# Kernel optimization log

Measured on AMD Instinct MI355X. Metric: run time of the kernel, lower is better.

## Reference

```python
import jax, jax.numpy as jnp
import numpy as np

B, S, D, H = 4, 2048, 512, 8
HD = D // H  # head dim = 64


def setup_inputs() -> dict:
    key = jax.random.key(0)
    ks = jax.random.split(key, 7)
    s = 0.02
    return {
        "X": jax.random.normal(ks[0], (B, S, D), dtype=jnp.float32),
        "Y": jax.random.normal(ks[1], (B, S, D), dtype=jnp.float32),
        "Z": jax.random.normal(ks[2], (B, S, D), dtype=jnp.float32),
        # weights stored as [in, out] (torch Linear weight transposed)
        "Wq": jax.random.normal(ks[3], (D, D), dtype=jnp.float32) * s,
        "Wk": jax.random.normal(ks[4], (D, D), dtype=jnp.float32) * s,
        "Wv": jax.random.normal(ks[5], (D, D), dtype=jnp.float32) * s,  # dead in original forward
        "Wo": jax.random.normal(ks[6], (D, D), dtype=jnp.float32) * s,
    }


def _split_heads(t):
    # [B, S, D] -> [B, H, S, HD]
    return t.reshape(B, S, H, HD).transpose(0, 2, 1, 3)


def reference(X, Y, Z, Wq, Wk, Wv, Wo):
    q = _split_heads(X @ Wq)
    k = _split_heads(Y @ Wk)
    # NOTE: original module (faithfully) uses W_o for the value projection; W_v is unused.
    v = _split_heads(Z @ Wo)
    scores = jnp.einsum("bhqd,bhkd->bhqk", q, k) / jnp.sqrt(jnp.float32(HD))
    # sigmoid(s) > 0.5  <=>  s > 0 (sigmoid strictly monotone); keep score else 0
    scores = jnp.where(scores > 0, scores, jnp.float32(0))
    attn = jax.nn.softmax(scores, axis=-1)
    out = jnp.einsum("bhqk,bhkd->bhqd", attn, v)  # dropout inactive at eval
    out = out.transpose(0, 2, 1, 3).reshape(B, S, D)  # merge heads
    return out @ Wo
```

## Files before the change

kernel.cpp:

```cpp
#include <hip/hip_runtime.h>
#include <math.h>

#define S_LEN 2048
#define DIM   512
#define M_TOT 8192
#define NCH   (S_LEN / 64)

typedef __attribute__((ext_vector_type(8))) short bf16x8;
typedef __attribute__((ext_vector_type(4))) short bf16x4;
typedef __attribute__((ext_vector_type(4))) float f32x4;
typedef __attribute__((ext_vector_type(16))) float f32x16;

#define MFMA(a, b, c)   __builtin_amdgcn_mfma_f32_16x16x32_bf16((a), (b), (c), 0, 0, 0)
#define MFMA32(a, b, c) __builtin_amdgcn_mfma_f32_32x32x16_bf16((a), (b), (c), 0, 0, 0)

#define QSCALE 0.18033688011112042f

__device__ __forceinline__ short f2b(float x) {
    union { float f; unsigned u; } v; v.f = x;
    unsigned r = v.u + 0x7FFFu + ((v.u >> 16) & 1u);
    return (short)(r >> 16);
}

__device__ __forceinline__ unsigned cvtpk(float a, float b) {
    unsigned r;
    asm("v_cvt_pk_bf16_f32 %0, %1, %2" : "=v"(r) : "v"(a), "v"(b));
    return r;
}

__device__ __forceinline__ bf16x8 cvt8(float4 lo, float4 hi) {
    union { unsigned u[4]; bf16x8 v; } o;
    o.u[0] = cvtpk(lo.x, lo.y);
    o.u[1] = cvtpk(lo.z, lo.w);
    o.u[2] = cvtpk(hi.x, hi.y);
    o.u[3] = cvtpk(hi.z, hi.w);
    return o.v;
}

__device__ __forceinline__ float fast_exp2(float x) {
#if __has_builtin(__builtin_amdgcn_exp2f)
    return __builtin_amdgcn_exp2f(x);
#else
    return __expf(x * 0.693147180559945f);
#endif
}

__global__ __launch_bounds__(256) void prep_wt(const float* Wq, const float* Wk, const float* Wo,
                                               short* Wtq, short* Wtk, short* Wto) {
    const int zi = blockIdx.z;
    const float* W = zi == 0 ? Wq : zi == 1 ? Wk : Wo;
    short*      Wt = zi == 0 ? Wtq : zi == 1 ? Wtk : Wto;
    const float sc = zi == 0 ? QSCALE : 1.0f;
    __shared__ short Ts[64 * 72];
    const int t = threadIdx.x;
    const int k0 = blockIdx.x * 64, n0 = blockIdx.y * 64;
    #pragma unroll
    for (int it = 0; it < 4; ++it) {
        const int r = (t >> 4) + 16 * it;
        const int cq = t & 15;
        float4 v = *(const float4*)&W[(size_t)(k0 + r) * DIM + n0 + cq * 4];
        Ts[(4 * cq + 0) * 72 + r] = f2b(v.x * sc);
        Ts[(4 * cq + 1) * 72 + r] = f2b(v.y * sc);
        Ts[(4 * cq + 2) * 72 + r] = f2b(v.z * sc);
        Ts[(4 * cq + 3) * 72 + r] = f2b(v.w * sc);
    }
    __syncthreads();
    #pragma unroll
    for (int it = 0; it < 2; ++it) {
        const int n = (t >> 3) + 32 * it;
        const int sg = t & 7;
        *(bf16x8*)&Wt[(size_t)(n0 + n) * DIM + k0 + sg * 8] = *(const bf16x8*)&Ts[n * 72 + sg * 8];
    }
}

__global__ __launch_bounds__(256) void proj_gemm(const float* __restrict__ X,
                                                 const float* __restrict__ Y,
                                                 const float* __restrict__ Z,
                                                 const short* __restrict__ Wtq,
                                                 const short* __restrict__ Wtk,
                                                 const short* __restrict__ Wto,
                                                 short* __restrict__ Qb,
                                                 short* __restrict__ Kb,
                                                 short* __restrict__ Vt) {
    const int zi = blockIdx.z;
    const float* A  = zi == 0 ? X : zi == 1 ? Y : Z;
    const short* Bw = zi == 0 ? Wtq : zi == 1 ? Wtk : Wto;

    __shared__ short As[128 * 40];
    __shared__ short Bs[128 * 40];
    const int tid = threadIdx.x;
    const int w = tid >> 6, ln = tid & 63, l15 = ln & 15, quad = ln >> 4;
    const int m0 = blockIdx.x * 128, n0 = blockIdx.y * 128;
    const int wm = (w & 1) * 64, wn = (w >> 1) * 64;

    const int r0 = tid >> 2, r1 = r0 + 64;
    const int sg = tid & 3;
    const float* ap0 = A  + (size_t)(m0 + r0) * DIM + sg * 8;
    const float* ap1 = A  + (size_t)(m0 + r1) * DIM + sg * 8;
    const short* bp0 = Bw + (size_t)(n0 + r0) * DIM + sg * 8;
    const short* bp1 = Bw + (size_t)(n0 + r1) * DIM + sg * 8;

    float4 a0l = *(const float4*)ap0, a0h = *(const float4*)(ap0 + 4);
    float4 a1l = *(const float4*)ap1, a1h = *(const float4*)(ap1 + 4);
    bf16x8 b0 = *(const bf16x8*)bp0, b1 = *(const bf16x8*)bp1;

    f32x4 acc[4][4] = {};

    for (int k0 = 0; k0 < DIM; k0 += 32) {
        __syncthreads();
        *(bf16x8*)&As[r0 * 40 + sg * 8] = cvt8(a0l, a0h);
        *(bf16x8*)&As[r1 * 40 + sg * 8] = cvt8(a1l, a1h);
        *(bf16x8*)&Bs[r0 * 40 + sg * 8] = b0;
        *(bf16x8*)&Bs[r1 * 40 + sg * 8] = b1;
        __syncthreads();
        const int kn = (k0 + 32 < DIM) ? k0 + 32 : 0;
        a0l = *(const float4*)(ap0 + kn); a0h = *(const float4*)(ap0 + kn + 4);
        a1l = *(const float4*)(ap1 + kn); a1h = *(const float4*)(ap1 + kn + 4);
        b0 = *(const bf16x8*)(bp0 + kn); b1 = *(const bf16x8*)(bp1 + kn);

        bf16x8 af[4], bf[4];
        #pragma unroll
        for (int mf = 0; mf < 4; ++mf) af[mf] = *(const bf16x8*)&As[(wm + 16 * mf + l15) * 40 + quad * 8];
        #pragma unroll
        for (int nf = 0; nf < 4; ++nf) bf[nf] = *(const bf16x8*)&Bs[(wn + 16 * nf + l15) * 40 + quad * 8];
        #pragma unroll
        for (int mf = 0; mf < 4; ++mf)
            #pragma unroll
            for (int nf = 0; nf < 4; ++nf)
                acc[mf][nf] = MFMA(af[mf], bf[nf], acc[mf][nf]);
    }

    if (zi < 2) {
        short* C = zi == 0 ? Qb : Kb;
        #pragma unroll
        for (int mf = 0; mf < 4; ++mf)
            #pragma unroll
            for (int nf = 0; nf < 4; ++nf)
                #pragma unroll
                for (int r = 0; r < 4; ++r)
                    C[(size_t)(m0 + wm + 16 * mf + 4 * quad + r) * DIM + n0 + wn + 16 * nf + l15] =
                        f2b(acc[mf][nf][r]);
    } else {
        #pragma unroll
        for (int mf = 0; mf < 4; ++mf)
            #pragma unroll
            for (int nf = 0; nf < 4; ++nf) {
                const int col = n0 + wn + 16 * nf + l15;
                const int h = col >> 6, hd = col & 63;
                const int row0_ = m0 + wm + 16 * mf + 4 * quad;
                const int bb = row0_ >> 11, s0 = row0_ & 2047;
                bf16x4 o = { f2b(acc[mf][nf][0]), f2b(acc[mf][nf][1]),
                             f2b(acc[mf][nf][2]), f2b(acc[mf][nf][3]) };
                *(bf16x4*)&Vt[((size_t)((bb * 8 + h) * 64 + hd)) * S_LEN + s0] = o;
            }
    }
}

__global__ __launch_bounds__(256) void out_gemm(const short* __restrict__ Ob,
                                                const short* __restrict__ Wto,
                                                float* __restrict__ Cout) {
    __shared__ short As[64 * 40];
    __shared__ short Bs[64 * 40];
    const int tid = threadIdx.x;
    const int w = tid >> 6, ln = tid & 63, l15 = ln & 15, quad = ln >> 4;

    const int f = blockIdx.x;
    const int swz = ((f & 7) << 7) | (f >> 3);
    const int m0 = (swz >> 3) * 64, n0 = (swz & 7) * 64;
    const int wm = (w & 1) * 32, wn = (w >> 1) * 32;

    const int row = tid >> 2;
    const int sg = tid & 3;
    const short* ap = Ob  + (size_t)(m0 + row) * DIM + sg * 8;
    const short* bp = Wto + (size_t)(n0 + row) * DIM + sg * 8;

    bf16x8 a0 = *(const bf16x8*)ap, b0 = *(const bf16x8*)bp;

    f32x4 acc[2][2] = {};

    for (int k0 = 0; k0 < DIM; k0 += 32) {
        __syncthreads();
        *(bf16x8*)&As[row * 40 + sg * 8] = a0;
        *(bf16x8*)&Bs[row * 40 + sg * 8] = b0;
        __syncthreads();
        const int kn = (k0 + 32 < DIM) ? k0 + 32 : 0;
        a0 = *(const bf16x8*)(ap + kn); b0 = *(const bf16x8*)(bp + kn);

        bf16x8 af[2], bf[2];
        #pragma unroll
        for (int mf = 0; mf < 2; ++mf) af[mf] = *(const bf16x8*)&As[(wm + 16 * mf + l15) * 40 + quad * 8];
        #pragma unroll
        for (int nf = 0; nf < 2; ++nf) bf[nf] = *(const bf16x8*)&Bs[(wn + 16 * nf + l15) * 40 + quad * 8];
        #pragma unroll
        for (int mf = 0; mf < 2; ++mf)
            #pragma unroll
            for (int nf = 0; nf < 2; ++nf)
                acc[mf][nf] = MFMA(af[mf], bf[nf], acc[mf][nf]);
    }
    #pragma unroll
    for (int mf = 0; mf < 2; ++mf)
        #pragma unroll
        for (int nf = 0; nf < 2; ++nf)
            #pragma unroll
            for (int r = 0; r < 4; ++r)
                Cout[(size_t)(m0 + wm + 16 * mf + 4 * quad + r) * DIM + n0 + wn + 16 * nf + l15] =
                    acc[mf][nf][r];
}

__global__ __launch_bounds__(256) void attn_mfma(const short* __restrict__ Qb,
                                                 const short* __restrict__ Kb,
                                                 const short* __restrict__ Vtg,
                                                 short* __restrict__ Ob) {
    __shared__ short Ks[2][64 * 72];
    __shared__ short Vs[2][64 * 72];
    __shared__ float Ds[4][32];

    const int tid = threadIdx.x;
    const int w = tid >> 6, ln = tid & 63, n31 = ln & 31, hL = ln >> 5;

    const int f = blockIdx.x;
    const int swz = ((f & 7) << 6) | (f >> 3);
    const int qt0 = (swz & 15) * 128;
    const int bh  = swz >> 4;
    const int b = bh >> 3, h = bh & 7;
    const size_t tokbase = (size_t)b * S_LEN;

    const int q0w = qt0 + 32 * w;
    bf16x8 qf[4];
    #pragma unroll
    for (int dk = 0; dk < 4; ++dk)
        qf[dk] = *(const bf16x8*)&Qb[(tokbase + q0w + n31) * DIM + h * 64 + 16 * dk + 8 * hL];

    const int srow = tid >> 2, sg = tid & 3;
    const short* kbase = Kb  + (tokbase + srow) * DIM + h * 64 + sg * 16;
    const short* vbase = Vtg + ((size_t)bh * 64 + srow) * S_LEN;

    union b8split { bf16x8 v; struct { bf16x4 lo, hi; } s; };

    bf16x8 kr0, kr1;
    b8split vrA, vrB;

    f32x16 oacc[2] = {};
    f32x4 d4 = {0.f, 0.f, 0.f, 0.f};

    kr0 = *(const bf16x8*)kbase;       kr1 = *(const bf16x8*)(kbase + 8);
    vrA.v = *(const bf16x8*)(vbase + 8 * sg);
    vrB.v = *(const bf16x8*)(vbase + 32 + 8 * sg);
    *(bf16x8*)&Ks[0][srow * 72 + sg * 16]     = kr0;
    *(bf16x8*)&Ks[0][srow * 72 + sg * 16 + 8] = kr1;
    {
        short* vrow = &Vs[0][srow * 72 + 16 * sg];
        *(bf16x4*)&vrow[0]  = vrA.s.lo;  *(bf16x4*)&vrow[8]  = vrA.s.hi;
        *(bf16x4*)&vrow[4]  = vrB.s.lo;  *(bf16x4*)&vrow[12] = vrB.s.hi;
    }
    kr0 = *(const bf16x8*)(kbase + (size_t)64 * DIM);
    kr1 = *(const bf16x8*)(kbase + (size_t)64 * DIM + 8);
    vrA.v = *(const bf16x8*)(vbase + 64 + 8 * sg);
    vrB.v = *(const bf16x8*)(vbase + 64 + 32 + 8 * sg);
    __syncthreads();

    for (int kc = 0; kc < NCH; ++kc) {
        const int cur = kc & 1;
        if (kc + 1 < NCH) {
            *(bf16x8*)&Ks[cur ^ 1][srow * 72 + sg * 16]     = kr0;
            *(bf16x8*)&Ks[cur ^ 1][srow * 72 + sg * 16 + 8] = kr1;
            short* vrow = &Vs[cur ^ 1][srow * 72 + 16 * sg];
            *(bf16x4*)&vrow[0]  = vrA.s.lo;  *(bf16x4*)&vrow[8]  = vrA.s.hi;
            *(bf16x4*)&vrow[4]  = vrB.s.lo;  *(bf16x4*)&vrow[12] = vrB.s.hi;
        }
        if (kc + 2 < NCH) {
            const size_t ko = (size_t)(kc + 2) * 64 * DIM;
            const size_t vo = (size_t)(kc + 2) * 64;
            kr0 = *(const bf16x8*)(kbase + ko);
            kr1 = *(const bf16x8*)(kbase + ko + 8);
            vrA.v = *(const bf16x8*)(vbase + vo + 8 * sg);
            vrB.v = *(const bf16x8*)(vbase + vo + 32 + 8 * sg);
        }

        f32x16 sacc[2] = {};
        __builtin_amdgcn_s_setprio(1);
        #pragma unroll
        for (int kt = 0; kt < 2; ++kt)
            #pragma unroll
            for (int dk = 0; dk < 4; ++dk) {
                bf16x8 ka = *(const bf16x8*)&Ks[cur][(32 * kt + n31) * 72 + 16 * dk + 8 * hL];
                sacc[kt] = MFMA32(ka, qf[dk], sacc[kt]);
            }
        __builtin_amdgcn_s_setprio(0);

        unsigned cp[16];
        #pragma unroll
        for (int kt = 0; kt < 2; ++kt)
            #pragma unroll
            for (int p = 0; p < 8; ++p) {
                const float e0 = fast_exp2(fmaxf(sacc[kt][2 * p], 0.f));
                const float e1 = fast_exp2(fmaxf(sacc[kt][2 * p + 1], 0.f));
                d4[p & 3] += e0 + e1;
                cp[8 * kt + p] = cvtpk(e0, e1);
            }

        __builtin_amdgcn_s_setprio(1);
        #pragma unroll
        for (int m = 0; m < 4; ++m) {
            union { unsigned u[4]; bf16x8 v; } pu;
            pu.u[0] = cp[2 * m];     pu.u[1] = cp[2 * m + 1];
            pu.u[2] = cp[2 * m + 8]; pu.u[3] = cp[2 * m + 9];
            #pragma unroll
            for (int nt = 0; nt < 2; ++nt) {
                bf16x8 vb = *(const bf16x8*)&Vs[cur][(32 * nt + n31) * 72 + 16 * m + 8 * hL];
                oacc[nt] = MFMA32(pu.v, vb, oacc[nt]);
            }
        }
        __builtin_amdgcn_s_setprio(0);
        __syncthreads();
    }

    float dtot = (d4[0] + d4[1]) + (d4[2] + d4[3]);
    dtot += __shfl_xor(dtot, 32);
    const float dinv = 1.0f / dtot;
    if (ln < 32) Ds[w][n31] = dinv;
    __syncthreads();
    f32x4 dv[4];
    #pragma unroll
    for (int g = 0; g < 4; ++g)
        dv[g] = *(const f32x4*)&Ds[w][8 * g + 4 * hL];

    #pragma unroll
    for (int nt = 0; nt < 2; ++nt)
        #pragma unroll
        for (int r = 0; r < 16; ++r) {
            const int qb = 32 * w + 4 * hL + 8 * (r >> 2) + (r & 3);
            Ob[(tokbase + qt0 + qb) * DIM + h * 64 + 32 * nt + n31] =
                f2b(oacc[nt][r] * dv[r >> 2][r & 3]);
        }
}

extern "C" void kernel_launch(void* const* d_in, const int* in_sizes, int n_in,
                              void* d_out, int out_size, void* d_ws, size_t ws_size,
                              hipStream_t stream) {
    const float* X  = (const float*)d_in[0];
    const float* Y  = (const float*)d_in[1];
    const float* Z  = (const float*)d_in[2];
    const float* Wq = (const float*)d_in[3];
    const float* Wk = (const float*)d_in[4];
    const float* Wo = (const float*)d_in[6];

    char* p = (char*)d_ws;
    const size_t MD = (size_t)M_TOT * DIM;
    short* Qb  = (short*)p; p += MD * 2;
    short* Kb  = (short*)p; p += MD * 2;
    short* Vt  = (short*)p; p += MD * 2;
    short* Ob  = (short*)p; p += MD * 2;
    short* Wtq = (short*)p; p += (size_t)DIM * DIM * 2;
    short* Wtk = (short*)p; p += (size_t)DIM * DIM * 2;
    short* Wto = (short*)p; p += (size_t)DIM * DIM * 2;

    prep_wt<<<dim3(8, 8, 3), 256, 0, stream>>>(Wq, Wk, Wo, Wtq, Wtk, Wto);
    proj_gemm<<<dim3(64, 4, 3), 256, 0, stream>>>(X, Y, Z, Wtq, Wtk, Wto, Qb, Kb, Vt);
    attn_mfma<<<dim3(512), 256, 0, stream>>>(Qb, Kb, Vt, Ob);
    out_gemm<<<dim3(1024), 256, 0, stream>>>(Ob, Wto, (float*)d_out);
}
```

Before: 193.7 us.

## Retile projection GEMM to 64-row by full-width 512-column blocks

```diff
diff --git a/kernel.cpp b/kernel.cpp
--- a/kernel.cpp
+++ b/kernel.cpp
@@ -82,52 +82,54 @@
                                                  short* __restrict__ Qb,
                                                  short* __restrict__ Kb,
                                                  short* __restrict__ Vt) {
-    const int zi = blockIdx.z;
+    const int zi = blockIdx.y;
     const float* A  = zi == 0 ? X : zi == 1 ? Y : Z;
     const short* Bw = zi == 0 ? Wtq : zi == 1 ? Wtk : Wto;
 
-    __shared__ short As[128 * 40];
-    __shared__ short Bs[128 * 40];
+    __shared__ short As[64 * 40];
+    __shared__ short Bs[512 * 40];
     const int tid = threadIdx.x;
     const int w = tid >> 6, ln = tid & 63, l15 = ln & 15, quad = ln >> 4;
-    const int m0 = blockIdx.x * 128, n0 = blockIdx.y * 128;
-    const int wm = (w & 1) * 64, wn = (w >> 1) * 64;
-
-    const int r0 = tid >> 2, r1 = r0 + 64;
+    const int m0 = blockIdx.x * 64;
+    const int wn = w * 128;
+
+    const int r0 = tid >> 2;
     const int sg = tid & 3;
-    const float* ap0 = A  + (size_t)(m0 + r0) * DIM + sg * 8;
-    const float* ap1 = A  + (size_t)(m0 + r1) * DIM + sg * 8;
-    const short* bp0 = Bw + (size_t)(n0 + r0) * DIM + sg * 8;
-    const short* bp1 = Bw + (size_t)(n0 + r1) * DIM + sg * 8;
-
-    float4 a0l = *(const float4*)ap0, a0h = *(const float4*)(ap0 + 4);
-    float4 a1l = *(const float4*)ap1, a1h = *(const float4*)(ap1 + 4);
-    bf16x8 b0 = *(const bf16x8*)bp0, b1 = *(const bf16x8*)bp1;
-
-    f32x4 acc[4][4] = {};
+    const float* ap = A + (size_t)(m0 + r0) * DIM + sg * 8;
+    const short* bp = Bw + (size_t)r0 * DIM + sg * 8;
+
+    float4 a0l = *(const float4*)ap, a0h = *(const float4*)(ap + 4);
+    bf16x8 br[8];
+    #pragma unroll
+    for (int i = 0; i < 8; ++i)
+        br[i] = *(const bf16x8*)(bp + (size_t)(64 * i) * DIM);
+
+    f32x4 acc[4][8] = {};
 
     for (int k0 = 0; k0 < DIM; k0 += 32) {
         __syncthreads();
         *(bf16x8*)&As[r0 * 40 + sg * 8] = cvt8(a0l, a0h);
-        *(bf16x8*)&As[r1 * 40 + sg * 8] = cvt8(a1l, a1h);
-        *(bf16x8*)&Bs[r0 * 40 + sg * 8] = b0;
-        *(bf16x8*)&Bs[r1 * 40 + sg * 8] = b1;
+        #pragma unroll
+        for (int i = 0; i < 8; ++i)
+            *(bf16x8*)&Bs[(r0 + 64 * i) * 40 + sg * 8] = br[i];
         __syncthreads();
         const int kn = (k0 + 32 < DIM) ? k0 + 32 : 0;
-        a0l = *(const float4*)(ap0 + kn); a0h = *(const float4*)(ap0 + kn + 4);
-        a1l = *(const float4*)(ap1 + kn); a1h = *(const float4*)(ap1 + kn + 4);
-        b0 = *(const bf16x8*)(bp0 + kn); b1 = *(const bf16x8*)(bp1 + kn);
-
-        bf16x8 af[4], bf[4];
-        #pragma unroll
-        for (int mf = 0; mf < 4; ++mf) af[mf] = *(const bf16x8*)&As[(wm + 16 * mf + l15) * 40 + quad * 8];
-        #pragma unroll
-        for (int nf = 0; nf < 4; ++nf) bf[nf] = *(const bf16x8*)&Bs[(wn + 16 * nf + l15) * 40 + quad * 8];
+        a0l = *(const float4*)(ap + kn); a0h = *(const float4*)(ap + kn + 4);
+        #pragma unroll
+        for (int i = 0; i < 8; ++i)
+            br[i] = *(const bf16x8*)(bp + (size_t)(64 * i) * DIM + kn);
+
+        bf16x8 af[4];
         #pragma unroll
         for (int mf = 0; mf < 4; ++mf)
-            #pragma unroll
-            for (int nf = 0; nf < 4; ++nf)
-                acc[mf][nf] = MFMA(af[mf], bf[nf], acc[mf][nf]);
+            af[mf] = *(const bf16x8*)&As[(16 * mf + l15) * 40 + quad * 8];
+        #pragma unroll
+        for (int nf = 0; nf < 8; ++nf) {
+            bf16x8 bfr = *(const bf16x8*)&Bs[(wn + 16 * nf + l15) * 40 + quad * 8];
+            #pragma unroll
+            for (int mf = 0; mf < 4; ++mf)
+                acc[mf][nf] = MFMA(af[mf], bfr, acc[mf][nf]);
+        }
     }
 
     if (zi < 2) {
@@ -135,19 +137,19 @@
         #pragma unroll
         for (int mf = 0; mf < 4; ++mf)
             #pragma unroll
-            for (int nf = 0; nf < 4; ++nf)
+            for (int nf = 0; nf < 8; ++nf)
                 #pragma unroll
                 for (int r = 0; r < 4; ++r)
-                    C[(size_t)(m0 + wm + 16 * mf + 4 * quad + r) * DIM + n0 + wn + 16 * nf + l15] =
+                    C[(size_t)(m0 + 16 * mf + 4 * quad + r) * DIM + wn + 16 * nf + l15] =
                         f2b(acc[mf][nf][r]);
     } else {
         #pragma unroll
         for (int mf = 0; mf < 4; ++mf)
             #pragma unroll
-            for (int nf = 0; nf < 4; ++nf) {
-                const int col = n0 + wn + 16 * nf + l15;
+            for (int nf = 0; nf < 8; ++nf) {
+                const int col = wn + 16 * nf + l15;
                 const int h = col >> 6, hd = col & 63;
-                const int row0_ = m0 + wm + 16 * mf + 4 * quad;
+                const int row0_ = m0 + 16 * mf + 4 * quad;
                 const int bb = row0_ >> 11, s0 = row0_ & 2047;
                 bf16x4 o = { f2b(acc[mf][nf][0]), f2b(acc[mf][nf][1]),
                              f2b(acc[mf][nf][2]), f2b(acc[mf][nf][3]) };
@@ -356,7 +358,7 @@
     short* Wto = (short*)p; p += (size_t)DIM * DIM * 2;
 
     prep_wt<<<dim3(8, 8, 3), 256, 0, stream>>>(Wq, Wk, Wo, Wtq, Wtk, Wto);
-    proj_gemm<<<dim3(64, 4, 3), 256, 0, stream>>>(X, Y, Z, Wtq, Wtk, Wto, Qb, Kb, Vt);
+    proj_gemm<<<dim3(128, 3), 256, 0, stream>>>(X, Y, Z, Wtq, Wtk, Wto, Qb, Kb, Vt);
     attn_mfma<<<dim3(512), 256, 0, stream>>>(Qb, Kb, Vt, Ob);
     out_gemm<<<dim3(1024), 256, 0, stream>>>(Ob, Wto, (float*)d_out);
 }
```

Measured after the change: 197.9 us. 1.02x slower.
